# Kernel optimization log

Measured on AMD Instinct MI355X. Metric: run time of the kernel, lower is better.

Reference implementation:

```python
import jax, jax.numpy as jnp
import numpy as np

B, NQ, N, D_IN, D_KEY, D_MODEL = 8, 2048, 2048, 512, 512, 512


def setup_inputs() -> dict:
    key = jax.random.key(0)
    k1, k2, k3, k4, k5, k6 = jax.random.split(key, 6)
    lim_k = np.sqrt(6.0 / (D_IN + D_KEY))
    lim_v = np.sqrt(6.0 / (D_IN + D_MODEL))
    return {
        "node_features": jax.random.normal(k1, (B, N, D_IN), dtype=jnp.float32),
        "query": jax.random.normal(k2, (B, NQ, D_IN), dtype=jnp.float32),
        "mask": jax.random.bernoulli(k3, 0.3, (NQ, B, N)),  # True = masked out
        "wq": jax.random.uniform(k4, (D_IN, D_KEY), jnp.float32, -lim_k, lim_k),
        "wk": jax.random.uniform(k5, (D_IN, D_KEY), jnp.float32, -lim_k, lim_k),
        "wv": jax.random.uniform(k6, (D_IN, D_MODEL), jnp.float32, -lim_v, lim_v),
    }


def reference(node_features, query, mask, wq, wk, wv):
    # Projections
    Q = query @ wq              # [B, NQ, d_key]
    K = node_features @ wk      # [B, N, d_key]
    V = node_features @ wv      # [B, N, d_model]
    # Raw scores [B, NQ, N]
    scores = jnp.einsum("bqd,bnd->bqn", Q, K)
    b, nq, n = scores.shape
    # Faithful to tf: reshape to (NQ, B, N), mask with float32.min, reshape back
    s = scores.reshape(nq, b, n)
    masked = jnp.where(mask, jnp.finfo(jnp.float32).min, s).reshape(b, nq, n)
    # Scale AFTER masking (as in the original), then softmax over keys
    attn = jax.nn.softmax(masked / jnp.sqrt(jnp.float32(K.shape[-1])), axis=-1)
    return attn @ V             # [B, NQ, d_model]
```

## Files before the change

### kernel.cpp

```cpp
#include <hip/hip_runtime.h>

#define BATCH 8
#define NQ    2048
#define NKV   2048
#define DIN   512
#define DKEY  512
#define DMOD  512

typedef __attribute__((ext_vector_type(8))) short bf16x8;
typedef __attribute__((ext_vector_type(4))) float f32x4;

__device__ __forceinline__ unsigned short f2bf(float f) {
  unsigned int u = __builtin_bit_cast(unsigned int, f);
  u += 0x7fffu + ((u >> 16) & 1u);
  return (unsigned short)(u >> 16);
}

#define GLD16(gp, lp) __builtin_amdgcn_global_load_lds( \
    (const __attribute__((address_space(1))) unsigned int*)(gp), \
    (__attribute__((address_space(3))) unsigned int*)(lp), 16, 0, 0)

__global__ void detect_mode(const unsigned int* __restrict__ mask, int* __restrict__ flag) {
  __shared__ int c1s;
  if (threadIdx.x == 0) c1s = 0;
  __syncthreads();
  int c1 = 0;
  for (int i = threadIdx.x; i < 16384; i += 256) {
    unsigned int u = mask[i];
    if (u & 0x0000ff00u) c1++;
  }
  atomicAdd(&c1s, c1);
  __syncthreads();
  if (threadIdx.x == 0) *flag = (c1s > 0) ? 1 : 4;
}

__global__ __launch_bounds__(256) void pack_mask(
    const unsigned char* __restrict__ m, const int* __restrict__ flag,
    unsigned long long* __restrict__ pm)
{
  const int g = blockIdx.x * 256 + threadIdx.x;
  const size_t base = (size_t)g * 64;
  unsigned long long bits = 0;
  if (*flag == 1) {
    const uint4* p = (const uint4*)(m + base);
#pragma unroll
    for (int j = 0; j < 4; ++j) {
      uint4 v = p[j];
      unsigned int w[4] = {v.x, v.y, v.z, v.w};
#pragma unroll
      for (int q = 0; q < 4; ++q) {
        unsigned int u = w[q];
#pragma unroll
        for (int b = 0; b < 4; ++b)
          if ((u >> (8 * b)) & 0xffu) bits |= 1ull << (j * 16 + q * 4 + b);
      }
    }
  } else {
    const uint4* p = (const uint4*)(m + base * 4);
#pragma unroll
    for (int j = 0; j < 16; ++j) {
      uint4 v = p[j];
      if (v.x) bits |= 1ull << (j * 4 + 0);
      if (v.y) bits |= 1ull << (j * 4 + 1);
      if (v.z) bits |= 1ull << (j * 4 + 2);
      if (v.w) bits |= 1ull << (j * 4 + 3);
    }
  }
  pm[g] = bits;
}

__global__ void cvt_two(const float* __restrict__ a, const float* __restrict__ b,
                        unsigned short* __restrict__ oa, unsigned short* __restrict__ ob) {
  int i = blockIdx.x * 256 + threadIdx.x;
  const float* src;
  unsigned short* dst;
  int j;
  if (i < 2097152) { src = a; dst = oa; j = i; }
  else             { src = b; dst = ob; j = i - 2097152; }
  float4 v = ((const float4*)src)[j];
  ushort4 o;
  o.x = f2bf(v.x); o.y = f2bf(v.y); o.z = f2bf(v.z); o.w = f2bf(v.w);
  ((ushort4*)dst)[j] = o;
}

__global__ void cvt_w3(const float* __restrict__ wq, const float* __restrict__ wk,
                       const float* __restrict__ wv,
                       unsigned short* __restrict__ oq, unsigned short* __restrict__ ok,
                       unsigned short* __restrict__ ov) {
  int idx = blockIdx.x * 256 + threadIdx.x;
  int w = idx >> 18;
  int rem = idx & 262143;
  int n = rem >> 9, k = rem & 511;
  const float* W = (w == 0) ? wq : (w == 1) ? wk : wv;
  unsigned short* O = (w == 0) ? oq : (w == 1) ? ok : ov;
  O[n * 512 + k] = f2bf(W[k * 512 + n]);
}

__device__ __forceinline__ void gemm256_core(
    const unsigned short* __restrict__ Ab,
    const unsigned short* __restrict__ Bb,
    unsigned short* __restrict__ C,
    long ldA, long ldB, long ldO, int nk, long bm, long bn, char* smem,
    const unsigned long long* __restrict__ pmask)
{
  const int tid = threadIdx.x;
  const int lane = tid & 63;
  const int wid = tid >> 6;
  const int wr = wid >> 1;
  const int wc = wid & 1;
  const int fr = lane & 15, fq = lane >> 4;

  const int srow = tid >> 3;
  const int clog = (tid & 7) ^ (srow & 7);

  char* buf0 = smem;
  char* buf1 = smem + 65536;

  f32x4 acc[4][8] = {};

  const int swz0 = ((fq)     ^ (fr & 7)) * 16;
  const int swz1 = ((4 + fq) ^ (fr & 7)) * 16;
  const int arow = (wr * 64 + fr) * 128;
  const int brow = (wc * 128 + fr) * 128;

  {
    const unsigned short* ga = Ab + (bm + srow) * ldA + clog * 8;
    const unsigned short* gb = Bb + (bn + srow) * ldB + clog * 8;
#pragma unroll
    for (int l = 0; l < 4; ++l) {
      GLD16(ga + (long)l * 64 * ldA, buf0 + l * 8192 + tid * 16);
      GLD16(gb + (long)l * 64 * ldB, buf0 + 32768 + l * 8192 + tid * 16);
    }
  }

  char* cur = buf0;
  char* nxt = buf1;
  for (int t = 0; t < nk; ++t) {
    __builtin_amdgcn_sched_barrier(0);
    __builtin_amdgcn_s_barrier();
    if (t + 1 < nk) {
      const long k0 = (long)(t + 1) * 64;
      const unsigned short* ga = Ab + (bm + srow) * ldA + k0 + clog * 8;
      const unsigned short* gb = Bb + (bn + srow) * ldB + k0 + clog * 8;
#pragma unroll
      for (int l = 0; l < 4; ++l) {
        GLD16(ga + (long)l * 64 * ldA, nxt + l * 8192 + tid * 16);
        GLD16(gb + (long)l * 64 * ldB, nxt + 32768 + l * 8192 + tid * 16);
      }
      asm volatile("s_waitcnt vmcnt(8)" ::: "memory");
    } else {
      asm volatile("s_waitcnt vmcnt(0)" ::: "memory");
    }
    __builtin_amdgcn_s_barrier();
    __builtin_amdgcn_sched_barrier(0);

    const char* bufA = cur;
    const char* bufB = cur + 32768;
#pragma unroll
    for (int kh = 0; kh < 2; ++kh) {
      const int swz = kh ? swz1 : swz0;
      bf16x8 a[4];
#pragma unroll
      for (int mi = 0; mi < 4; ++mi)
        a[mi] = *(const bf16x8*)(bufA + arow + mi * 2048 + swz);
#pragma unroll
      for (int nh = 0; nh < 2; ++nh) {
        bf16x8 b[4];
#pragma unroll
        for (int nj = 0; nj < 4; ++nj)
          b[nj] = *(const bf16x8*)(bufB + brow + (nh * 4 + nj) * 2048 + swz);
        __builtin_amdgcn_s_setprio(1);
#pragma unroll
        for (int mi = 0; mi < 4; ++mi)
#pragma unroll
          for (int nj = 0; nj < 4; ++nj)
            acc[mi][nh * 4 + nj] = __builtin_amdgcn_mfma_f32_16x16x32_bf16(
                a[mi], b[nj], acc[mi][nh * 4 + nj], 0, 0, 0);
        __builtin_amdgcn_s_setprio(0);
      }
    }
    char* tmp = cur; cur = nxt; nxt = tmp;
  }

  const float SCALE = 0.04419417382415922f;
  if (pmask == nullptr) {
#pragma unroll
    for (int mi = 0; mi < 4; ++mi)
#pragma unroll
      for (int ni = 0; ni < 8; ++ni) {
        const long row = bm + wr * 64 + mi * 16 + fq * 4;
        const long col = bn + wc * 128 + ni * 16 + fr;
#pragma unroll
        for (int r = 0; r < 4; ++r)
          C[(row + r) * ldO + col] = f2bf(acc[mi][ni][r]);
      }
  } else {
    const long wbase = (bn >> 6) + wc * 2;
#pragma unroll
    for (int mi = 0; mi < 4; ++mi) {
      const long rowb = bm + wr * 64 + mi * 16 + fq * 4;
#pragma unroll
      for (int r = 0; r < 4; ++r) {
        const long row = rowb + r;
        const unsigned long long w0 = pmask[row * 32 + wbase];
        const unsigned long long w1 = pmask[row * 32 + wbase + 1];
        unsigned short* Crow = C + row * ldO + bn + wc * 128 + fr;
#pragma unroll
        for (int ni = 0; ni < 8; ++ni) {
          const unsigned long long w = (ni < 4) ? w0 : w1;
          const int sh = (ni & 3) * 16 + fr;
          float e = ((w >> sh) & 1ull) ? 0.0f : __expf(acc[mi][ni][r] * SCALE);
          Crow[ni * 16] = f2bf(e);
        }
      }
    }
  }
}

__global__ __launch_bounds__(512, 2) void gemm256_scores(
    const unsigned short* __restrict__ Q, const unsigned short* __restrict__ Kb,
    unsigned short* __restrict__ S, const unsigned long long* __restrict__ pm)
{
  extern __shared__ char smem[];
  const long z = blockIdx.z;
  gemm256_core(Q + z * 1048576, Kb + z * 1048576, S + z * 4194304,
               512, 512, 2048, 8, (long)blockIdx.x * 256, (long)blockIdx.y * 256, smem,
               pm + z * 65536);
}

__global__ __launch_bounds__(512, 2) void gemm256_proj(
    const unsigned short* __restrict__ Xq, const unsigned short* __restrict__ Xn,
    const unsigned short* __restrict__ Wqt, const unsigned short* __restrict__ Wkt,
    const unsigned short* __restrict__ Wvt,
    unsigned short* __restrict__ Q, unsigned short* __restrict__ Kb,
    unsigned short* __restrict__ Vt)
{
  extern __shared__ char smem[];
  const int z = blockIdx.z;
  if (z == 0)
    gemm256_core(Xq, Wqt, Q, 512, 512, 512, 8,
                 (long)blockIdx.x * 256, (long)blockIdx.y * 256, smem, nullptr);
  else if (z == 1)
    gemm256_core(Xn, Wkt, Kb, 512, 512, 512, 8,
                 (long)blockIdx.x * 256, (long)blockIdx.y * 256, smem, nullptr);
  else
    gemm256_core(Wvt, Xn, Vt, 512, 512, 16384, 8,
                 (long)blockIdx.y * 256, (long)blockIdx.x * 256, smem, nullptr);
}

__global__ __launch_bounds__(256) void rowsum_inv(
    const unsigned short* __restrict__ E, float* __restrict__ inv)
{
  const int row = blockIdx.x * 4 + (threadIdx.x >> 6);
  const int lane = threadIdx.x & 63;
  const uint4* p = (const uint4*)(E + (size_t)row * 2048);
  float s = 0.f;
#pragma unroll
  for (int j = 0; j < 4; ++j) {
    uint4 v = p[lane + j * 64];
    unsigned int w[4] = {v.x, v.y, v.z, v.w};
#pragma unroll
    for (int q = 0; q < 4; ++q) {
      s += __builtin_bit_cast(float, (w[q] & 0xffffu) << 16);
      s += __builtin_bit_cast(float, w[q] & 0xffff0000u);
    }
  }
#pragma unroll
  for (int off = 32; off > 0; off >>= 1) s += __shfl_xor(s, off);
  if (lane == 0) inv[row] = 1.0f / s;
}

__global__ __launch_bounds__(512, 2) void gemm_pv(
    const unsigned short* __restrict__ E, const unsigned short* __restrict__ Vt,
    const float* __restrict__ inv, float* __restrict__ O)
{
  extern __shared__ char smem[];
  const long z = blockIdx.z;
  const unsigned short* Ab = E + z * 4194304;
  const unsigned short* Bb = Vt + z * 2048;
  const long bm = (long)blockIdx.x * 256;
  const long bn = (long)blockIdx.y * 128;

  const int tid = threadIdx.x;
  const int lane = tid & 63;
  const int wid = tid >> 6;
  const int wr = wid >> 1;
  const int wc = wid & 1;
  const int fr = lane & 15, fq = lane >> 4;

  const int srow = tid >> 3;
  const int clog = (tid & 7) ^ (srow & 7);

  char* buf0 = smem;
  char* buf1 = smem + 49152;

  f32x4 acc[4][4] = {};

  const int swz0 = ((fq)     ^ (fr & 7)) * 16;
  const int swz1 = ((4 + fq) ^ (fr & 7)) * 16;
  const int arow = (wr * 64 + fr) * 128;
  const int brow = (wc * 64 + fr) * 128;

  {
    const unsigned short* ga = Ab + (bm + srow) * 2048 + clog * 8;
    const unsigned short* gb = Bb + (bn + srow) * 16384 + clog * 8;
#pragma unroll
    for (int l = 0; l < 4; ++l)
      GLD16(ga + (long)l * 64 * 2048, buf0 + l * 8192 + tid * 16);
#pragma unroll
    for (int l = 0; l < 2; ++l)
      GLD16(gb + (long)l * 64 * 16384, buf0 + 32768 + l * 8192 + tid * 16);
  }

  char* cur = buf0;
  char* nxt = buf1;
  for (int t = 0; t < 32; ++t) {
    __builtin_amdgcn_sched_barrier(0);
    __builtin_amdgcn_s_barrier();
    if (t + 1 < 32) {
      const long k0 = (long)(t + 1) * 64;
      const unsigned short* ga = Ab + (bm + srow) * 2048 + k0 + clog * 8;
      const unsigned short* gb = Bb + (bn + srow) * 16384 + k0 + clog * 8;
#pragma unroll
      for (int l = 0; l < 4; ++l)
        GLD16(ga + (long)l * 64 * 2048, nxt + l * 8192 + tid * 16);
#pragma unroll
      for (int l = 0; l < 2; ++l)
        GLD16(gb + (long)l * 64 * 16384, nxt + 32768 + l * 8192 + tid * 16);
      asm volatile("s_waitcnt vmcnt(6)" ::: "memory");
    } else {
      asm volatile("s_waitcnt vmcnt(0)" ::: "memory");
    }
    __builtin_amdgcn_s_barrier();
    __builtin_amdgcn_sched_barrier(0);

    const char* bufA = cur;
    const char* bufB = cur + 32768;
#pragma unroll
    for (int kh = 0; kh < 2; ++kh) {
      const int swz = kh ? swz1 : swz0;
      bf16x8 a[4], b[4];
#pragma unroll
      for (int mi = 0; mi < 4; ++mi)
        a[mi] = *(const bf16x8*)(bufA + arow + mi * 2048 + swz);
#pragma unroll
      for (int nj = 0; nj < 4; ++nj)
        b[nj] = *(const bf16x8*)(bufB + brow + nj * 2048 + swz);
      __builtin_amdgcn_s_setprio(1);
#pragma unroll
      for (int mi = 0; mi < 4; ++mi)
#pragma unroll
        for (int nj = 0; nj < 4; ++nj)
          acc[mi][nj] = __builtin_amdgcn_mfma_f32_16x16x32_bf16(
              a[mi], b[nj], acc[mi][nj], 0, 0, 0);
      __builtin_amdgcn_s_setprio(0);
    }
    char* tmp = cur; cur = nxt; nxt = tmp;
  }

  float* Ob = O + z * 1048576;
  const float* invb = inv + z * 2048;
#pragma unroll
  for (int mi = 0; mi < 4; ++mi)
#pragma unroll
    for (int nj = 0; nj < 4; ++nj) {
      const long row = bm + wr * 64 + mi * 16 + fq * 4;
      const long col = bn + wc * 64 + nj * 16 + fr;
#pragma unroll
      for (int r = 0; r < 4; ++r)
        Ob[(row + r) * 512 + col] = acc[mi][nj][r] * invb[row + r];
    }
}

extern "C" void kernel_launch(void* const* d_in, const int* in_sizes, int n_in,
                              void* d_out, int out_size, void* d_ws, size_t ws_size,
                              hipStream_t stream) {
  const float* node  = (const float*)d_in[0];
  const float* query = (const float*)d_in[1];
  const unsigned char* mask = (const unsigned char*)d_in[2];
  const float* wq = (const float*)d_in[3];
  const float* wk = (const float*)d_in[4];
  const float* wv = (const float*)d_in[5];
  float* out = (float*)d_out;

  char* ws = (char*)d_ws;
  unsigned short* Q   = (unsigned short*)(ws);
  unsigned short* Kb  = (unsigned short*)(ws + 16777216);
  unsigned short* Vt  = (unsigned short*)(ws + 33554432);
  unsigned short* E   = (unsigned short*)(ws + 50331648);
  unsigned short* Xq  = (unsigned short*)(ws + 50331648);
  unsigned short* Xn  = (unsigned short*)(ws + 50331648 + 16777216);
  unsigned short* Wqt = (unsigned short*)(ws + 50331648 + 33554432);
  unsigned short* Wkt = Wqt + 262144;
  unsigned short* Wvt = Wkt + 262144;
  float* inv = (float*)(ws + 117440512);
  int* flag  = (int*)(ws + 117506048);
  unsigned long long* pm = (unsigned long long*)(ws + 118489088);

  detect_mode<<<1, 256, 0, stream>>>((const unsigned int*)mask, flag);
  pack_mask<<<2048, 256, 0, stream>>>(mask, flag, pm);

  cvt_two<<<16384, 256, 0, stream>>>(query, node, Xq, Xn);
  cvt_w3<<<3072, 256, 0, stream>>>(wq, wk, wv, Wqt, Wkt, Wvt);

  dim3 gp(64, 2, 3);
  gemm256_proj<<<gp, 512, 131072, stream>>>(Xq, Xn, Wqt, Wkt, Wvt, Q, Kb, Vt);

  dim3 gs(8, 8, 8);
  gemm256_scores<<<gs, 512, 131072, stream>>>(Q, Kb, E, pm);

  rowsum_inv<<<4096, 256, 0, stream>>>(E, inv);

  dim3 gv(8, 4, 8);
  gemm_pv<<<gv, 512, 98304, stream>>>(E, Vt, inv, out);
}
```

Baseline: 219.7 us.

## Fuse softmax row sums into scores epilogue and narrow projection tiles

Row sums of the exponentiated scores are now accumulated in the scores GEMM epilogue via shuffle reduction and atomicAdd into a zeroed buffer. This removes the separate rowsum pass that re-read the whole bf16 score matrix. The projection GEMM switches to 256x128 tiles with more blocks, and the PV GEMM reuses a shared narrow core. The narrow core's PV epilogue now computes the reciprocal of each row sum itself. The change also adds workgroup barriers before the MFMA blocks and sets launch bounds to one block per CU. The cost is atomic contention, an extra memset, and possibly lower occupancy.

```diff
diff --git a/kernel.cpp b/kernel.cpp
--- a/kernel.cpp
+++ b/kernel.cpp
@@ -1,11 +1,4 @@
 #include <hip/hip_runtime.h>
-
-#define BATCH 8
-#define NQ    2048
-#define NKV   2048
-#define DIN   512
-#define DKEY  512
-#define DMOD  512
 
 typedef __attribute__((ext_vector_type(8))) short bf16x8;
 typedef __attribute__((ext_vector_type(4))) float f32x4;
@@ -96,12 +89,135 @@
   O[n * 512 + k] = f2bf(W[k * 512 + n]);
 }
 
-__device__ __forceinline__ void gemm256_core(
+__global__ __launch_bounds__(512, 1) void gemm256_scores(
+    const unsigned short* __restrict__ Qg, const unsigned short* __restrict__ Kg,
+    unsigned short* __restrict__ Sg, const unsigned long long* __restrict__ pm,
+    float* __restrict__ sums)
+{
+  extern __shared__ char smem[];
+  const long z = blockIdx.z;
+  const unsigned short* Ab = Qg + z * 1048576;
+  const unsigned short* Bb = Kg + z * 1048576;
+  unsigned short* C = Sg + z * 4194304;
+  const unsigned long long* pmask = pm + z * 65536;
+  float* sumz = sums + z * 2048;
+  const long bm = (long)blockIdx.x * 256;
+  const long bn = (long)blockIdx.y * 256;
+
+  const int tid = threadIdx.x;
+  const int lane = tid & 63;
+  const int wid = tid >> 6;
+  const int wr = wid >> 1;
+  const int wc = wid & 1;
+  const int fr = lane & 15, fq = lane >> 4;
+  const int srow = tid >> 3;
+  const int clog = (tid & 7) ^ (srow & 7);
+
+  char* buf0 = smem;
+  char* buf1 = smem + 65536;
+
+  f32x4 acc[4][8] = {};
+
+  const int swz0 = ((fq)     ^ (fr & 7)) * 16;
+  const int swz1 = ((4 + fq) ^ (fr & 7)) * 16;
+  const int arow = (wr * 64 + fr) * 128;
+  const int brow = (wc * 128 + fr) * 128;
+
+  {
+    const unsigned short* ga = Ab + (bm + srow) * 512 + clog * 8;
+    const unsigned short* gb = Bb + (bn + srow) * 512 + clog * 8;
+#pragma unroll
+    for (int l = 0; l < 4; ++l) {
+      GLD16(ga + (long)l * 64 * 512, buf0 + l * 8192 + tid * 16);
+      GLD16(gb + (long)l * 64 * 512, buf0 + 32768 + l * 8192 + tid * 16);
+    }
+  }
+
+  char* cur = buf0;
+  char* nxt = buf1;
+  for (int t = 0; t < 8; ++t) {
+    __builtin_amdgcn_sched_barrier(0);
+    __builtin_amdgcn_s_barrier();
+    if (t < 7) {
+      const long k0 = (long)(t + 1) * 64;
+      const unsigned short* ga = Ab + (bm + srow) * 512 + k0 + clog * 8;
+      const unsigned short* gb = Bb + (bn + srow) * 512 + k0 + clog * 8;
+#pragma unroll
+      for (int l = 0; l < 4; ++l) {
+        GLD16(ga + (long)l * 64 * 512, nxt + l * 8192 + tid * 16);
+        GLD16(gb + (long)l * 64 * 512, nxt + 32768 + l * 8192 + tid * 16);
+      }
+      asm volatile("s_waitcnt vmcnt(8)" ::: "memory");
+    } else {
+      asm volatile("s_waitcnt vmcnt(0)" ::: "memory");
+    }
+    __builtin_amdgcn_s_barrier();
+    __builtin_amdgcn_sched_barrier(0);
+
+    const char* bufA = cur;
+    const char* bufB = cur + 32768;
+#pragma unroll
+    for (int kh = 0; kh < 2; ++kh) {
+      const int swz = kh ? swz1 : swz0;
+      bf16x8 a[4];
+#pragma unroll
+      for (int mi = 0; mi < 4; ++mi)
+        a[mi] = *(const bf16x8*)(bufA + arow + mi * 2048 + swz);
+#pragma unroll
+      for (int nh = 0; nh < 2; ++nh) {
+        bf16x8 b[4];
+#pragma unroll
+        for (int nj = 0; nj < 4; ++nj)
+          b[nj] = *(const bf16x8*)(bufB + brow + (nh * 4 + nj) * 2048 + swz);
+        __builtin_amdgcn_sched_barrier(0);
+        __builtin_amdgcn_s_barrier();
+        __builtin_amdgcn_s_setprio(1);
+#pragma unroll
+        for (int mi = 0; mi < 4; ++mi)
+#pragma unroll
+          for (int nj = 0; nj < 4; ++nj)
+            acc[mi][nh * 4 + nj] = __builtin_amdgcn_mfma_f32_16x16x32_bf16(
+                a[mi], b[nj], acc[mi][nh * 4 + nj], 0, 0, 0);
+        __builtin_amdgcn_s_setprio(0);
+        __builtin_amdgcn_sched_barrier(0);
+      }
+    }
+    char* tmp = cur; cur = nxt; nxt = tmp;
+  }
+
+  const float SCALE = 0.04419417382415922f;
+  const long wbase = (bn >> 6) + wc * 2;
+#pragma unroll
+  for (int mi = 0; mi < 4; ++mi) {
+    const long rowb = bm + wr * 64 + mi * 16 + fq * 4;
+#pragma unroll
+    for (int r = 0; r < 4; ++r) {
+      const long row = rowb + r;
+      const unsigned long long w0 = pmask[row * 32 + wbase];
+      const unsigned long long w1 = pmask[row * 32 + wbase + 1];
+      unsigned short* Crow = C + row * 2048 + bn + wc * 128 + fr;
+      float s = 0.f;
+#pragma unroll
+      for (int ni = 0; ni < 8; ++ni) {
+        const unsigned long long w = (ni < 4) ? w0 : w1;
+        const int sh = (ni & 3) * 16 + fr;
+        float e = ((w >> sh) & 1ull) ? 0.0f : __expf(acc[mi][ni][r] * SCALE);
+        s += e;
+        Crow[ni * 16] = f2bf(e);
+      }
+      s += __shfl_xor(s, 1); s += __shfl_xor(s, 2);
+      s += __shfl_xor(s, 4); s += __shfl_xor(s, 8);
+      if (fr == 0) atomicAdd(&sumz[row], s);
+    }
+  }
+}
+
+__device__ __forceinline__ void gemm_narrow_core(
     const unsigned short* __restrict__ Ab,
     const unsigned short* __restrict__ Bb,
-    unsigned short* __restrict__ C,
+    void* __restrict__ Cb,
     long ldA, long ldB, long ldO, int nk, long bm, long bn, char* smem,
-    const unsigned long long* __restrict__ pmask)
+    int mode, const float* __restrict__ sumz)
 {
   const int tid = threadIdx.x;
   const int lane = tid & 63;
@@ -109,28 +225,28 @@
   const int wr = wid >> 1;
   const int wc = wid & 1;
   const int fr = lane & 15, fq = lane >> 4;
-
   const int srow = tid >> 3;
   const int clog = (tid & 7) ^ (srow & 7);
 
   char* buf0 = smem;
-  char* buf1 = smem + 65536;
-
-  f32x4 acc[4][8] = {};
+  char* buf1 = smem + 49152;
+
+  f32x4 acc[4][4] = {};
 
   const int swz0 = ((fq)     ^ (fr & 7)) * 16;
   const int swz1 = ((4 + fq) ^ (fr & 7)) * 16;
   const int arow = (wr * 64 + fr) * 128;
-  const int brow = (wc * 128 + fr) * 128;
+  const int brow = (wc * 64 + fr) * 128;
 
   {
     const unsigned short* ga = Ab + (bm + srow) * ldA + clog * 8;
     const unsigned short* gb = Bb + (bn + srow) * ldB + clog * 8;
 #pragma unroll
-    for (int l = 0; l < 4; ++l) {
+    for (int l = 0; l < 4; ++l)
       GLD16(ga + (long)l * 64 * ldA, buf0 + l * 8192 + tid * 16);
+#pragma unroll
+    for (int l = 0; l < 2; ++l)
       GLD16(gb + (long)l * 64 * ldB, buf0 + 32768 + l * 8192 + tid * 16);
-    }
   }
 
   char* cur = buf0;
@@ -143,11 +259,12 @@
       const unsigned short* ga = Ab + (bm + srow) * ldA + k0 + clog * 8;
       const unsigned short* gb = Bb + (bn + srow) * ldB + k0 + clog * 8;
 #pragma unroll
-      for (int l = 0; l < 4; ++l) {
+      for (int l = 0; l < 4; ++l)
         GLD16(ga + (long)l * 64 * ldA, nxt + l * 8192 + tid * 16);
+#pragma unroll
+      for (int l = 0; l < 2; ++l)
         GLD16(gb + (long)l * 64 * ldB, nxt + 32768 + l * 8192 + tid * 16);
-      }
-      asm volatile("s_waitcnt vmcnt(8)" ::: "memory");
+      asm volatile("s_waitcnt vmcnt(6)" ::: "memory");
     } else {
       asm volatile("s_waitcnt vmcnt(0)" ::: "memory");
     }
@@ -159,76 +276,59 @@
 #pragma unroll
     for (int kh = 0; kh < 2; ++kh) {
       const int swz = kh ? swz1 : swz0;
-      bf16x8 a[4];
+      bf16x8 a[4], b[4];
 #pragma unroll
       for (int mi = 0; mi < 4; ++mi)
         a[mi] = *(const bf16x8*)(bufA + arow + mi * 2048 + swz);
 #pragma unroll
-      for (int nh = 0; nh < 2; ++nh) {
-        bf16x8 b[4];
+      for (int nj = 0; nj < 4; ++nj)
+        b[nj] = *(const bf16x8*)(bufB + brow + nj * 2048 + swz);
+      __builtin_amdgcn_sched_barrier(0);
+      __builtin_amdgcn_s_barrier();
+      __builtin_amdgcn_s_setprio(1);
+#pragma unroll
+      for (int mi = 0; mi < 4; ++mi)
 #pragma unroll
         for (int nj = 0; nj < 4; ++nj)
-          b[nj] = *(const bf16x8*)(bufB + brow + (nh * 4 + nj) * 2048 + swz);
-        __builtin_amdgcn_s_setprio(1);
-#pragma unroll
-        for (int mi = 0; mi < 4; ++mi)
-#pragma unroll
-          for (int nj = 0; nj < 4; ++nj)
-            acc[mi][nh * 4 + nj] = __builtin_amdgcn_mfma_f32_16x16x32_bf16(
-                a[mi], b[nj], acc[mi][nh * 4 + nj], 0, 0, 0);
-        __builtin_amdgcn_s_setprio(0);
-      }
+          acc[mi][nj] = __builtin_amdgcn_mfma_f32_16x16x32_bf16(
+              a[mi], b[nj], acc[mi][nj], 0, 0, 0);
+      __builtin_amdgcn_s_setprio(0);
+      __builtin_amdgcn_sched_barrier(0);
     }
     char* tmp = cur; cur = nxt; nxt = tmp;
   }
 
-  const float SCALE = 0.04419417382415922f;
-  if (pmask == nullptr) {
+  if (mode == 0) {
+    unsigned short* C = (unsigned short*)Cb;
 #pragma unroll
     for (int mi = 0; mi < 4; ++mi)
 #pragma unroll
-      for (int ni = 0; ni < 8; ++ni) {
+      for (int nj = 0; nj < 4; ++nj) {
         const long row = bm + wr * 64 + mi * 16 + fq * 4;
-        const long col = bn + wc * 128 + ni * 16 + fr;
+        const long col = bn + wc * 64 + nj * 16 + fr;
 #pragma unroll
         for (int r = 0; r < 4; ++r)
-          C[(row + r) * ldO + col] = f2bf(acc[mi][ni][r]);
+          C[(row + r) * ldO + col] = f2bf(acc[mi][nj][r]);
       }
   } else {
-    const long wbase = (bn >> 6) + wc * 2;
+    float* C = (float*)Cb;
 #pragma unroll
     for (int mi = 0; mi < 4; ++mi) {
       const long rowb = bm + wr * 64 + mi * 16 + fq * 4;
 #pragma unroll
       for (int r = 0; r < 4; ++r) {
         const long row = rowb + r;
-        const unsigned long long w0 = pmask[row * 32 + wbase];
-        const unsigned long long w1 = pmask[row * 32 + wbase + 1];
-        unsigned short* Crow = C + row * ldO + bn + wc * 128 + fr;
-#pragma unroll
-        for (int ni = 0; ni < 8; ++ni) {
-          const unsigned long long w = (ni < 4) ? w0 : w1;
-          const int sh = (ni & 3) * 16 + fr;
-          float e = ((w >> sh) & 1ull) ? 0.0f : __expf(acc[mi][ni][r] * SCALE);
-          Crow[ni * 16] = f2bf(e);
-        }
-      }
-    }
-  }
-}
-
-__global__ __launch_bounds__(512, 2) void gemm256_scores(
-    const unsigned short* __restrict__ Q, const unsigned short* __restrict__ Kb,
-    unsigned short* __restrict__ S, const unsigned long long* __restrict__ pm)
-{
-  extern __shared__ char smem[];
-  const long z = blockIdx.z;
-  gemm256_core(Q + z * 1048576, Kb + z * 1048576, S + z * 4194304,
-               512, 512, 2048, 8, (long)blockIdx.x * 256, (long)blockIdx.y * 256, smem,
-               pm + z * 65536);
-}
-
-__global__ __launch_bounds__(512, 2) void gemm256_proj(
+        const float iv = 1.0f / sumz[row];
+        const long colb = bn + wc * 64 + fr;
+#pragma unroll
+        for (int nj = 0; nj < 4; ++nj)
+          C[row * ldO + colb + nj * 16] = acc[mi][nj][r] * iv;
+      }
+    }
+  }
+}
+
+__global__ __launch_bounds__(512, 1) void gemm_proj(
     const unsigned short* __restrict__ Xq, const unsigned short* __restrict__ Xn,
     const unsigned short* __restrict__ Wqt, const unsigned short* __restrict__ Wkt,
     const unsigned short* __restrict__ Wvt,
@@ -237,139 +337,29 @@
 {
   extern __shared__ char smem[];
   const int z = blockIdx.z;
-  if (z == 0)
-    gemm256_core(Xq, Wqt, Q, 512, 512, 512, 8,
-                 (long)blockIdx.x * 256, (long)blockIdx.y * 256, smem, nullptr);
-  else if (z == 1)
-    gemm256_core(Xn, Wkt, Kb, 512, 512, 512, 8,
-                 (long)blockIdx.x * 256, (long)blockIdx.y * 256, smem, nullptr);
-  else
-    gemm256_core(Wvt, Xn, Vt, 512, 512, 16384, 8,
-                 (long)blockIdx.y * 256, (long)blockIdx.x * 256, smem, nullptr);
-}
-
-__global__ __launch_bounds__(256) void rowsum_inv(
-    const unsigned short* __restrict__ E, float* __restrict__ inv)
-{
-  const int row = blockIdx.x * 4 + (threadIdx.x >> 6);
-  const int lane = threadIdx.x & 63;
-  const uint4* p = (const uint4*)(E + (size_t)row * 2048);
-  float s = 0.f;
-#pragma unroll
-  for (int j = 0; j < 4; ++j) {
-    uint4 v = p[lane + j * 64];
-    unsigned int w[4] = {v.x, v.y, v.z, v.w};
-#pragma unroll
-    for (int q = 0; q < 4; ++q) {
-      s += __builtin_bit_cast(float, (w[q] & 0xffffu) << 16);
-      s += __builtin_bit_cast(float, w[q] & 0xffff0000u);
-    }
-  }
-#pragma unroll
-  for (int off = 32; off > 0; off >>= 1) s += __shfl_xor(s, off);
-  if (lane == 0) inv[row] = 1.0f / s;
-}
-
-__global__ __launch_bounds__(512, 2) void gemm_pv(
+  if (z == 0) {
+    gemm_narrow_core(Xq, Wqt, Q, 512, 512, 512, 8,
+                     (long)blockIdx.x * 256, (long)blockIdx.y * 128, smem, 0, nullptr);
+  } else if (z == 1) {
+    gemm_narrow_core(Xn, Wkt, Kb, 512, 512, 512, 8,
+                     (long)blockIdx.x * 256, (long)blockIdx.y * 128, smem, 0, nullptr);
+  } else {
+    const int flat = blockIdx.x * 4 + blockIdx.y;
+    gemm_narrow_core(Wvt, Xn, Vt, 512, 512, 16384, 8,
+                     (long)(flat >> 7) * 256, (long)(flat & 127) * 128, smem, 0, nullptr);
+  }
+}
+
+__global__ __launch_bounds__(512, 1) void gemm_pv(
     const unsigned short* __restrict__ E, const unsigned short* __restrict__ Vt,
-    const float* __restrict__ inv, float* __restrict__ O)
+    const float* __restrict__ sums, float* __restrict__ O)
 {
   extern __shared__ char smem[];
   const long z = blockIdx.z;
-  const unsigned short* Ab = E + z * 4194304;
-  const unsigned short* Bb = Vt + z * 2048;
-  const long bm = (long)blockIdx.x * 256;
-  const long bn = (long)blockIdx.y * 128;
-
-  const int tid = threadIdx.x;
-  const int lane = tid & 63;
-  const int wid = tid >> 6;
-  const int wr = wid >> 1;
-  const int wc = wid & 1;
-  const int fr = lane & 15, fq = lane >> 4;
-
-  const int srow = tid >> 3;
-  const int clog = (tid & 7) ^ (srow & 7);
-
-  char* buf0 = smem;
-  char* buf1 = smem + 49152;
-
-  f32x4 acc[4][4] = {};
-
-  const int swz0 = ((fq)     ^ (fr & 7)) * 16;
-  const int swz1 = ((4 + fq) ^ (fr & 7)) * 16;
-  const int arow = (wr * 64 + fr) * 128;
-  const int brow = (wc * 64 + fr) * 128;
-
-  {
-    const unsigned short* ga = Ab + (bm + srow) * 2048 + clog * 8;
-    const unsigned short* gb = Bb + (bn + srow) * 16384 + clog * 8;
-#pragma unroll
-    for (int l = 0; l < 4; ++l)
-      GLD16(ga + (long)l * 64 * 2048, buf0 + l * 8192 + tid * 16);
-#pragma unroll
-    for (int l = 0; l < 2; ++l)
-      GLD16(gb + (long)l * 64 * 16384, buf0 + 32768 + l * 8192 + tid * 16);
-  }
-
-  char* cur = buf0;
-  char* nxt = buf1;
-  for (int t = 0; t < 32; ++t) {
-    __builtin_amdgcn_sched_barrier(0);
-    __builtin_amdgcn_s_barrier();
-    if (t + 1 < 32) {
-      const long k0 = (long)(t + 1) * 64;
-      const unsigned short* ga = Ab + (bm + srow) * 2048 + k0 + clog * 8;
-      const unsigned short* gb = Bb + (bn + srow) * 16384 + k0 + clog * 8;
-#pragma unroll
-      for (int l = 0; l < 4; ++l)
-        GLD16(ga + (long)l * 64 * 2048, nxt + l * 8192 + tid * 16);
-#pragma unroll
-      for (int l = 0; l < 2; ++l)
-        GLD16(gb + (long)l * 64 * 16384, nxt + 32768 + l * 8192 + tid * 16);
-      asm volatile("s_waitcnt vmcnt(6)" ::: "memory");
-    } else {
-      asm volatile("s_waitcnt vmcnt(0)" ::: "memory");
-    }
-    __builtin_amdgcn_s_barrier();
-    __builtin_amdgcn_sched_barrier(0);
-
-    const char* bufA = cur;
-    const char* bufB = cur + 32768;
-#pragma unroll
-    for (int kh = 0; kh < 2; ++kh) {
-      const int swz = kh ? swz1 : swz0;
-      bf16x8 a[4], b[4];
-#pragma unroll
-      for (int mi = 0; mi < 4; ++mi)
-        a[mi] = *(const bf16x8*)(bufA + arow + mi * 2048 + swz);
-#pragma unroll
-      for (int nj = 0; nj < 4; ++nj)
-        b[nj] = *(const bf16x8*)(bufB + brow + nj * 2048 + swz);
-      __builtin_amdgcn_s_setprio(1);
-#pragma unroll
-      for (int mi = 0; mi < 4; ++mi)
-#pragma unroll
-        for (int nj = 0; nj < 4; ++nj)
-          acc[mi][nj] = __builtin_amdgcn_mfma_f32_16x16x32_bf16(
-              a[mi], b[nj], acc[mi][nj], 0, 0, 0);
-      __builtin_amdgcn_s_setprio(0);
-    }
-    char* tmp = cur; cur = nxt; nxt = tmp;
-  }
-
-  float* Ob = O + z * 1048576;
-  const float* invb = inv + z * 2048;
-#pragma unroll
-  for (int mi = 0; mi < 4; ++mi)
-#pragma unroll
-    for (int nj = 0; nj < 4; ++nj) {
-      const long row = bm + wr * 64 + mi * 16 + fq * 4;
-      const long col = bn + wc * 64 + nj * 16 + fr;
-#pragma unroll
-      for (int r = 0; r < 4; ++r)
-        Ob[(row + r) * 512 + col] = acc[mi][nj][r] * invb[row + r];
-    }
+  gemm_narrow_core(E + z * 4194304, Vt + z * 2048, O + z * 1048576,
+                   2048, 16384, 512, 32,
+                   (long)blockIdx.x * 256, (long)blockIdx.y * 128, smem,
+                   1, sums + z * 2048);
 }
 
 extern "C" void kernel_launch(void* const* d_in, const int* in_sizes, int n_in,
@@ -393,8 +383,8 @@
   unsigned short* Wqt = (unsigned short*)(ws + 50331648 + 33554432);
   unsigned short* Wkt = Wqt + 262144;
   unsigned short* Wvt = Wkt + 262144;
-  float* inv = (float*)(ws + 117440512);
-  int* flag  = (int*)(ws + 117506048);
+  float* sums = (float*)(ws + 117440512);
+  int* flag   = (int*)(ws + 117506048);
   unsigned long long* pm = (unsigned long long*)(ws + 118489088);
 
   detect_mode<<<1, 256, 0, stream>>>((const unsigned int*)mask, flag);
@@ -403,14 +393,13 @@
   cvt_two<<<16384, 256, 0, stream>>>(query, node, Xq, Xn);
   cvt_w3<<<3072, 256, 0, stream>>>(wq, wk, wv, Wqt, Wkt, Wvt);
 
-  dim3 gp(64, 2, 3);
-  gemm256_proj<<<gp, 512, 131072, stream>>>(Xq, Xn, Wqt, Wkt, Wvt, Q, Kb, Vt);
-
+  dim3 gp(64, 4, 3);
+  gemm_proj<<<gp, 512, 98304, stream>>>(Xq, Xn, Wqt, Wkt, Wvt, Q, Kb, Vt);
+
+  hipMemsetAsync(sums, 0, 65536, stream);
   dim3 gs(8, 8, 8);
-  gemm256_scores<<<gs, 512, 131072, stream>>>(Q, Kb, E, pm);
-
-  rowsum_inv<<<4096, 256, 0, stream>>>(E, inv);
+  gemm256_scores<<<gs, 512, 131072, stream>>>(Q, Kb, E, pm, sums);
 
   dim3 gv(8, 4, 8);
-  gemm_pv<<<gv, 512, 98304, stream>>>(E, Vt, inv, out);
-}
+  gemm_pv<<<gv, 512, 98304, stream>>>(E, Vt, sums, out);
+}
```

After: 219.1 us. No clear change (-0.3%).
